# Optimization experiments

Hardware: AMD Instinct MI355X
Metric: run time of the kernel (lower is better)

The kernel has to match this reference:

```python
import jax, jax.numpy as jnp
import numpy as np

# Dims (match init_kwargs): d_model=1024, H=16 heads, hd=64, lift=2 -> Nlift=128, top-k t=32
B, T, D = 1, 2048, 1024
H, HD, LIFT, TK = 16, 64, 2, 32
N = LIFT * HD  # 128 lifted dims per head
EPS = 1e-12


def topk_sparsify(x, k):
    """ReLU then keep only the top-k values per last-dim row (rest zeroed).
    Mathematically identical to the torch COO top-k construction: the sparse
    matrix equals the dense matrix with non-top-k entries zeroed."""
    x = jax.nn.relu(x)
    vals, idx = jax.lax.top_k(x, k)              # (..., k)
    n = x.shape[-1]
    flat_idx = idx.reshape(-1, k)
    flat_vals = vals.reshape(-1, k)
    R = flat_idx.shape[0]
    out = jnp.zeros((R, n), dtype=x.dtype)
    out = out.at[jnp.arange(R)[:, None], flat_idx].set(flat_vals)
    return out.reshape(x.shape)


def setup_inputs() -> dict:
    key = jax.random.key(0)
    ks = jax.random.split(key, 6)
    x = jax.random.normal(ks[0], (B, T, D), jnp.float32)
    W_q = jax.random.normal(ks[1], (H * N, D), jnp.float32) * 0.02
    W_k = jax.random.normal(ks[2], (H * N, D), jnp.float32) * 0.02
    W_v = jax.random.normal(ks[3], (H * HD, D), jnp.float32) * 0.02
    W_o = jax.random.normal(ks[4], (D, H * HD), jnp.float32) * 0.02
    sink = jax.random.normal(ks[5], (H, HD), jnp.float32) * 0.02
    log_beta = jnp.zeros((), jnp.float32)
    return {"x": x, "W_q": W_q, "W_k": W_k, "W_v": W_v, "W_o": W_o,
            "sink": sink, "log_beta": log_beta}


def reference(x, W_q, W_k, W_v, W_o, sink, log_beta):
    # Projections (Linear with no bias: x @ W.T)
    q = (x @ W_q.T).reshape(B, T, H, N)
    k = (x @ W_k.T).reshape(B, T, H, N)
    v = (x @ W_v.T).reshape(B, T, H, HD)

    # ReLU + top-k sparsification of lifted Q/K rows
    qs = topk_sparsify(q, TK).transpose(0, 2, 1, 3)  # (B,H,T,N)
    kk = topk_sparsify(k, TK).transpose(0, 2, 1, 3)  # (B,H,T,N)

    # A = Qs @ Ks^T per (batch, head) block; spspmm only produces same-block
    # entries, so the per-head batched matmul is the exact dense equivalent.
    A = jnp.einsum('bhin,bhjn->bhij', qs, kk)        # (B,H,T,T), all >= 0

    # Causal filter: keep j <= i
    causal = jnp.tril(jnp.ones((T, T), dtype=bool))
    A = jnp.where(causal, A, jnp.zeros((), A.dtype))

    # p=1 normalization with learned sink mass beta
    denom = A.sum(-1)                                # (B,H,T)
    beta = jnp.exp(log_beta)
    denom_ws = denom + beta
    A = A / jnp.maximum(denom_ws, EPS)[..., None]

    vh = v.transpose(0, 2, 1, 3)                     # (B,H,T,HD)
    Y = jnp.einsum('bhij,bhjd->bhid', A, vh)         # (B,H,T,HD)
    Y = Y + (beta / denom_ws)[..., None] * sink[None, :, None, :]

    Y = Y.transpose(0, 2, 1, 3).reshape(B, T, H * HD)
    return Y @ W_o.T
```

## Files before the change

### kernel.cpp

```cpp
#include <hip/hip_runtime.h>

typedef __attribute__((ext_vector_type(8))) short bf8v;
typedef __attribute__((ext_vector_type(4))) float f4v;
typedef unsigned short u16;
typedef unsigned int   u32;
#define AS1 __attribute__((address_space(1)))
#define AS3 __attribute__((address_space(3)))

__device__ inline u16 f2b(float f){
  u32 u = __builtin_bit_cast(u32, f);
  u += 0x7fffu + ((u >> 16) & 1u);
  return (u16)(u >> 16);
}

__global__ __launch_bounds__(256) void conv_all(const float* __restrict__ x,  const float* __restrict__ wq,
                                                const float* __restrict__ wk, const float* __restrict__ wv,
                                                const float* __restrict__ wo,
                                                u16* xb, u16* wqb, u16* wkb, u16* wvb, u16* wob){
  int i = blockIdx.x * 256 + threadIdx.x;
  const float* src; u16* dst; int off;
  if      (i <  524288){ src = x;  dst = xb;  off = i; }
  else if (i < 1048576){ src = wq; dst = wqb; off = i -  524288; }
  else if (i < 1572864){ src = wk; dst = wkb; off = i - 1048576; }
  else if (i < 1835008){ src = wv; dst = wvb; off = i - 1572864; }
  else                 { src = wo; dst = wob; off = i - 1835008; }
  float4 v = ((const float4*)src)[off];
  uint2 r;
  r.x = (u32)f2b(v.x) | ((u32)f2b(v.y) << 16);
  r.y = (u32)f2b(v.z) | ((u32)f2b(v.w) << 16);
  ((uint2*)dst)[off] = r;
}

template<int NFR>
__device__ __forceinline__ void gemm_core(const u16* __restrict__ A, const u16* __restrict__ B,
                                          int K, int m0, int n0, u16* lds, f4v (&acc)[4][NFR]){
  const int tid = threadIdx.x;
  const int l = tid & 63, w = tid >> 6;
  const int wrow = (w >> 1) * 64, wcol = (w & 1) * (NFR * 16);
  constexpr int SB = 4096 + NFR * 1024;
  #pragma unroll
  for (int a = 0; a < 4; a++)
    #pragma unroll
    for (int b = 0; b < NFR; b++) acc[a][b] = (f4v)0.0f;

  const int lrow = l >> 2;
  const int lseg = l & 3;

  auto stage = [&](int k0, int buf){
    u16* At = lds + buf * SB;
    u16* Bt = At + 4096;
    #pragma unroll
    for (int j = 0; j < 2; j++){
      int ca = w * 2 + j;
      int row = ca * 16 + lrow;
      int sseg = (lseg ^ ((row >> 1) & 3)) * 8;
      __builtin_amdgcn_global_load_lds((const AS1 void*)(A + (size_t)(m0 + row) * K + k0 + sseg),
                                       (AS3 void*)(At + ca * 512), 16, 0, 0);
    }
    #pragma unroll
    for (int j = 0; j < NFR / 2; j++){
      int cb = w * (NFR / 2) + j;
      int row = cb * 16 + lrow;
      int sseg = (lseg ^ ((row >> 1) & 3)) * 8;
      __builtin_amdgcn_global_load_lds((const AS1 void*)(B + (size_t)(n0 + row) * K + k0 + sseg),
                                       (AS3 void*)(Bt + cb * 512), 16, 0, 0);
    }
  };

  stage(0, 0);
  __syncthreads();
  int buf = 0;
  for (int k0 = 0; k0 < K; k0 += 32){
    if (k0 + 32 < K) stage(k0 + 32, buf ^ 1);
    const u16* At = lds + buf * SB;
    const u16* Bt = At + 4096;
    bf8v af[4], bfr[NFR];
    #pragma unroll
    for (int mr = 0; mr < 4; mr++){
      int row = wrow + mr * 16 + (l & 15);
      af[mr] = *(const bf8v*)(At + row * 32 + (((l >> 4) ^ ((row >> 1) & 3)) * 8));
    }
    #pragma unroll
    for (int nc = 0; nc < NFR; nc++){
      int row = wcol + nc * 16 + (l & 15);
      bfr[nc] = *(const bf8v*)(Bt + row * 32 + (((l >> 4) ^ ((row >> 1) & 3)) * 8));
    }
    #pragma unroll
    for (int mr = 0; mr < 4; mr++)
      #pragma unroll
      for (int nc = 0; nc < NFR; nc++)
        acc[mr][nc] = __builtin_amdgcn_mfma_f32_16x16x32_bf16(af[mr], bfr[nc], acc[mr][nc], 0, 0, 0);
    __syncthreads();
    buf ^= 1;
  }
}

__global__ __launch_bounds__(256, 4) void qkv_gemm(const u16* __restrict__ xb,
                                                   const u16* __restrict__ wqb, const u16* __restrict__ wkb,
                                                   const u16* __restrict__ wvb,
                                                   u16* qf, u16* kf, u16* vtb){
  __shared__ u16 lds[16384];
  int b = (blockIdx.x & 7) * 80 + (blockIdx.x >> 3);
  const u16* Bp; int which;
  if (b < 256)      { Bp = wqb; which = 0; }
  else if (b < 512) { Bp = wkb; which = 1; b -= 256; }
  else              { Bp = wvb; which = 2; b -= 512; }
  int sh = (which == 2) ? 3 : 4;
  int m0 = (b >> sh) * 128, n0 = (b & ((1 << sh) - 1)) * 128;

  f4v acc[4][4];
  gemm_core<4>(xb, Bp, 1024, m0, n0, lds, acc);

  const int l = threadIdx.x & 63, w = threadIdx.x >> 6;
  const int wrow = (w >> 1) * 64, wcol = (w & 1) * 64;
  if (which < 2){
    u16* C = which ? kf : qf;
    #pragma unroll
    for (int mr = 0; mr < 4; mr++)
      #pragma unroll
      for (int nc = 0; nc < 4; nc++)
        #pragma unroll
        for (int rr = 0; rr < 4; rr++){
          int row = m0 + wrow + mr * 16 + (l >> 4) * 4 + rr;
          int col = n0 + wcol + nc * 16 + (l & 15);
          C[(size_t)row * 2048 + col] = f2b(acc[mr][nc][rr]);
        }
  } else {
    #pragma unroll
    for (int mr = 0; mr < 4; mr++)
      #pragma unroll
      for (int nc = 0; nc < 4; nc++){
        int gcol = n0 + wcol + nc * 16 + (l & 15);
        int t0 = m0 + wrow + mr * 16 + (l >> 4) * 4;
        uint2 pk;
        pk.x = (u32)f2b(acc[mr][nc][0]) | ((u32)f2b(acc[mr][nc][1]) << 16);
        pk.y = (u32)f2b(acc[mr][nc][2]) | ((u32)f2b(acc[mr][nc][3]) << 16);
        *(uint2*)(vtb + (size_t)gcol * 2048 + t0) = pk;
      }
  }
}

__global__ __launch_bounds__(256, 4) void o_gemm(const u16* __restrict__ yb, const u16* __restrict__ wob,
                                                 float* out){
  __shared__ u16 lds[12288];
  int b = (blockIdx.x & 7) * 32 + (blockIdx.x >> 3);
  int m0 = (b >> 4) * 128, n0 = (b & 15) * 64;
  f4v acc[4][2];
  gemm_core<2>(yb, wob, 1024, m0, n0, lds, acc);
  const int l = threadIdx.x & 63, w = threadIdx.x >> 6;
  const int wrow = (w >> 1) * 64, wcol = (w & 1) * 32;
  #pragma unroll
  for (int mr = 0; mr < 4; mr++)
    #pragma unroll
    for (int nc = 0; nc < 2; nc++)
      #pragma unroll
      for (int rr = 0; rr < 4; rr++){
        int row = m0 + wrow + mr * 16 + (l >> 4) * 4 + rr;
        int col = n0 + wcol + nc * 16 + (l & 15);
        out[(size_t)row * 1024 + col] = acc[mr][nc][rr];
      }
}

__global__ __launch_bounds__(256) void topk2(const u16* __restrict__ qf, const u16* __restrict__ kf,
                                             u16* __restrict__ qsb, u16* __restrict__ ksb){
  int w = threadIdx.x >> 6, l = threadIdx.x & 63;
  int b = blockIdx.x;
  const u16* src; u16* dst;
  if (b < 2048){ src = qf; dst = qsb; } else { src = kf; dst = ksb; b -= 2048; }
  int base = b * 16 + w * 4;
  u32 u0[4], u1[4], pre[4];
  int tt[4], hh[4];
  #pragma unroll
  for (int j = 0; j < 4; j++){
    int r = base + j;
    tt[j] = r >> 4; hh[j] = r & 15;
    u32 pair = ((const u32*)(src + (size_t)tt[j] * 2048 + hh[j] * 128))[l];
    u0[j] = pair & 0xFFFFu; u1[j] = pair >> 16;
    if (u0[j] & 0x8000u) u0[j] = 0;
    if (u1[j] & 0x8000u) u1[j] = 0;
    pre[j] = 0;
  }
  for (int bb = 14; bb >= 0; --bb){
    #pragma unroll
    for (int j = 0; j < 4; j++){
      u32 cand = pre[j] | (1u << bb);
      int c = __builtin_popcountll(__ballot(u0[j] >= cand)) + __builtin_popcountll(__ballot(u1[j] >= cand));
      if (c >= 32) pre[j] = cand;
    }
  }
  #pragma unroll
  for (int j = 0; j < 4; j++){
    u32 o0 = (u0[j] >= pre[j]) ? u0[j] : 0u;
    u32 o1 = (u1[j] >= pre[j]) ? u1[j] : 0u;
    ((u32*)(dst + ((size_t)hh[j] * 2048 + tt[j]) * 128))[l] = o0 | (o1 << 16);
  }
}

__global__ __launch_bounds__(512, 6) void attn3(const u16* __restrict__ qs, const u16* __restrict__ ks,
                                                const u16* __restrict__ vt, const float* __restrict__ sink,
                                                const float* __restrict__ logbeta, u16* __restrict__ yout,
                                                float* __restrict__ Yp, float* __restrict__ Dp){
  __shared__ u16 Kt[8192];
  __shared__ u16 Vt[2][4096];
  __shared__ u16 St[8][16 * 72];
  const int tid = threadIdx.x, l = tid & 63, w = tid >> 6;
  const int b = blockIdx.x;
  const int slot = b >> 3;
  const int h = (b & 7) + 8 * (slot / 40);
  const int u = slot % 40;
  int it, chunk, nch;
  if (u < 4)       { it = u; chunk = 0; nch = 1; }
  else if (u < 12) { it = 4 + ((u - 4) >> 1);  chunk = (u - 4) & 1;  nch = 2; }
  else if (u < 24) { it = 8 + (u - 12) / 3;    chunk = (u - 12) % 3; nch = 3; }
  else             { it = 12 + ((u - 24) >> 2); chunk = (u - 24) & 3; nch = 4; }
  const int tiles = 2 * it + 2;
  const int jt0 = (tiles * chunk) / nch;
  const int jt1 = (tiles * (chunk + 1)) / nch;
  const int qrow0 = it * 128 + w * 16;
  const float beta = expf(logbeta[0]);

  bf8v qfr[4];
  {
    int trow = qrow0 + (l & 15);
    const u16* qrow = qs + ((size_t)h * 2048 + trow) * 128 + (l >> 4) * 8;
    #pragma unroll
    for (int kk = 0; kk < 4; kk++) qfr[kk] = *(const bf8v*)(qrow + kk * 32);
  }

  f4v accY[4];
  #pragma unroll
  for (int c = 0; c < 4; c++) accY[c] = (f4v)0.0f;
  float dsum[4] = {0.f, 0.f, 0.f, 0.f};

  const u16* kroot = ks + (size_t)h * 2048 * 128;
  const u16* vroot = vt + (size_t)h * 64 * 2048;

  auto stageK = [&](int jt){
    const u16* kbase = kroot + (size_t)jt * 64 * 128;
    #pragma unroll
    for (int i = 0; i < 2; i++){
      int g = i * 512 + tid;
      int r = g >> 4, c = g & 15;
      __builtin_amdgcn_global_load_lds((const AS1 void*)(kbase + r * 128 + (c ^ (r & 7)) * 8),
                                       (AS3 void*)(&Kt[(i * 512 + w * 64) * 8]), 16, 0, 0);
    }
  };
  auto stageV = [&](int jt, int b2){
    int d = tid >> 3, c = tid & 7;
    __builtin_amdgcn_global_load_lds((const AS1 void*)(vroot + (size_t)d * 2048 + jt * 64 + (c ^ (d & 7)) * 8),
                                     (AS3 void*)(&Vt[b2][w * 512]), 16, 0, 0);
  };

  stageK(jt0);
  stageV(jt0, 0);
  __syncthreads();
  int buf = 0;
  for (int jt = jt0; jt < jt1; ++jt){
    bool pf = (jt + 1 < jt1);
    if (pf) stageV(jt + 1, buf ^ 1);
    const bool act = (jt * 64 <= qrow0 + 15);

    f4v accS[4];
    if (act){
      #pragma unroll
      for (int c = 0; c < 4; c++) accS[c] = (f4v)0.0f;
      __builtin_amdgcn_s_setprio(1);
      #pragma unroll
      for (int c = 0; c < 4; c++){
        int r = c * 16 + (l & 15);
        #pragma unroll
        for (int kk = 0; kk < 4; kk++){
          int ch = kk * 4 + (l >> 4);
          bf8v kfr = *(const bf8v*)(&Kt[r * 128 + ((ch ^ (r & 7)) * 8)]);
          accS[c] = __builtin_amdgcn_mfma_f32_16x16x32_bf16(qfr[kk], kfr, accS[c], 0, 0, 0);
        }
      }
      __builtin_amdgcn_s_setprio(0);
    }
    __builtin_amdgcn_s_barrier();
    __builtin_amdgcn_sched_barrier(0);
    if (pf) stageK(jt + 1);

    if (act){
      if (jt * 64 + 63 > qrow0){
        #pragma unroll
        for (int c = 0; c < 4; c++)
          #pragma unroll
          for (int rr = 0; rr < 4; rr++){
            int i = qrow0 + (l >> 4) * 4 + rr;
            int j = jt * 64 + c * 16 + (l & 15);
            if (j > i) accS[c][rr] = 0.f;
          }
      }
      #pragma unroll
      for (int c = 0; c < 4; c++)
        #pragma unroll
        for (int rr = 0; rr < 4; rr++){
          dsum[rr] += accS[c][rr];
          St[w][((l >> 4) * 4 + rr) * 72 + c * 16 + (l & 15)] = f2b(accS[c][rr]);
        }
      __builtin_amdgcn_s_setprio(1);
      #pragma unroll
      for (int k2 = 0; k2 < 2; k2++){
        bf8v afr = *(const bf8v*)(&St[w][(l & 15) * 72 + k2 * 32 + (l >> 4) * 8]);
        #pragma unroll
        for (int c = 0; c < 4; c++){
          int d = c * 16 + (l & 15);
          int ch = k2 * 4 + (l >> 4);
          bf8v vfr = *(const bf8v*)(&Vt[buf][d * 64 + ((ch ^ (d & 7)) * 8)]);
          accY[c] = __builtin_amdgcn_mfma_f32_16x16x32_bf16(afr, vfr, accY[c], 0, 0, 0);
        }
      }
      __builtin_amdgcn_s_setprio(0);
    }
    __syncthreads();
    buf ^= 1;
  }

  #pragma unroll
  for (int rr = 0; rr < 4; rr++){
    float s = dsum[rr];
    s += __shfl_xor(s, 1, 64);
    s += __shfl_xor(s, 2, 64);
    s += __shfl_xor(s, 4, 64);
    s += __shfl_xor(s, 8, 64);
    dsum[rr] = s;
  }

  if (nch == 1){
    #pragma unroll
    for (int c = 0; c < 4; c++){
      float sv = sink[h * 64 + c * 16 + (l & 15)];
      #pragma unroll
      for (int rr = 0; rr < 4; rr++){
        float den = dsum[rr] + beta;
        float inv = 1.0f / fmaxf(den, 1e-12f);
        float y = (accY[c][rr] + beta * sv) * inv;
        int row = qrow0 + (l >> 4) * 4 + rr;
        yout[(size_t)row * 1024 + h * 64 + c * 16 + (l & 15)] = f2b(y);
      }
    }
  } else {
    float* yp = Yp + ((size_t)h * 40 + u) * 8192;
    #pragma unroll
    for (int c = 0; c < 4; c++)
      #pragma unroll
      for (int rr = 0; rr < 4; rr++){
        int rowib = w * 16 + (l >> 4) * 4 + rr;
        yp[rowib * 64 + c * 16 + (l & 15)] = accY[c][rr];
      }
    if ((l & 15) == 0){
      #pragma unroll
      for (int rr = 0; rr < 4; rr++)
        Dp[((size_t)h * 40 + u) * 128 + w * 16 + (l >> 4) * 4 + rr] = dsum[rr];
    }
  }
}

__global__ __launch_bounds__(256) void attn_reduce(const float* __restrict__ Yp, const float* __restrict__ Dp,
                                                   const float* __restrict__ sink, const float* __restrict__ logbeta,
                                                   u16* __restrict__ yout){
  int blk = blockIdx.x;
  int h = blk / 12, it = 4 + blk % 12;
  int nch = it / 4 + 1;
  int u0 = (it < 8) ? 4 + (it - 4) * 2 : (it < 12) ? 12 + (it - 8) * 3 : 24 + (it - 12) * 4;
  float beta = expf(logbeta[0]);
  __shared__ float inv_s[128];
  int t = threadIdx.x;
  if (t < 128){
    float s = 0.f;
    for (int c = 0; c < nch; c++) s += Dp[((size_t)h * 40 + u0 + c) * 128 + t];
    inv_s[t] = 1.0f / fmaxf(s + beta, 1e-12f);
  }
  __syncthreads();
  const float* base = Yp + ((size_t)h * 40 + u0) * 8192;
  #pragma unroll
  for (int e = 0; e < 32; e++){
    int idx = e * 256 + t;
    float acc = 0.f;
    for (int c = 0; c < nch; c++) acc += base[c * 8192 + idx];
    int row = idx >> 6, col = idx & 63;
    float y = (acc + beta * sink[h * 64 + col]) * inv_s[row];
    yout[(size_t)(it * 128 + row) * 1024 + h * 64 + col] = f2b(y);
  }
}

extern "C" void kernel_launch(void* const* d_in, const int* in_sizes, int n_in,
                              void* d_out, int out_size, void* d_ws, size_t ws_size,
                              hipStream_t stream){
  const float* x    = (const float*)d_in[0];
  const float* Wq   = (const float*)d_in[1];
  const float* Wk   = (const float*)d_in[2];
  const float* Wv   = (const float*)d_in[3];
  const float* Wo   = (const float*)d_in[4];
  const float* sink = (const float*)d_in[5];
  const float* logb = (const float*)d_in[6];

  char* ws = (char*)d_ws;
  u16*   xb  = (u16*)(ws + 0);
  u16*   wqb = (u16*)(ws + 4194304);
  u16*   wkb = (u16*)(ws + 8388608);
  u16*   wvb = (u16*)(ws + 12582912);
  u16*   wob = (u16*)(ws + 14680064);
  u16*   qf  = (u16*)(ws + 16777216);
  u16*   kf  = (u16*)(ws + 33554432);
  u16*   qsb = (u16*)(ws + 50331648);
  u16*   ksb = (u16*)(ws + 58720256);
  u16*   vtb = (u16*)(ws + 67108864);
  u16*   yb  = (u16*)(ws + 71303168);
  float* Yp  = (float*)(ws + 16777216);
  float* Dp  = (float*)(ws + 37748736);

  conv_all<<<8192, 256, 0, stream>>>(x, Wq, Wk, Wv, Wo, xb, wqb, wkb, wvb, wob);
  qkv_gemm<<<640, 256, 0, stream>>>(xb, wqb, wkb, wvb, qf, kf, vtb);
  topk2<<<4096, 256, 0, stream>>>(qf, kf, qsb, ksb);
  attn3<<<640, 512, 0, stream>>>(qsb, ksb, vtb, sink, logb, yb, Yp, Dp);
  attn_reduce<<<192, 256, 0, stream>>>(Yp, Dp, sink, logb, yb);
  o_gemm<<<256, 256, 0, stream>>>(yb, wob, (float*)d_out);
}
```

Measured before the change: 136.9 us.

## Fuse split-K attention reduction into attn3 via last-block atomic counter

Removes the separate attn_reduce kernel. Each split chunk block increments a per-(head, query tile) atomic counter after writing its partial Y and denominators, and the last block to arrive sums the partials, normalizes and writes bf16 output. The partial buffers are compacted to cover only split tiles, and a memset clears the counters each call. This saves a kernel launch and its scheduling gap, at the cost of thread fences, an atomic, and tail work done serially inside the attention kernel.

```diff
diff --git a/kernel.cpp b/kernel.cpp
--- a/kernel.cpp
+++ b/kernel.cpp
@@ -199,10 +199,13 @@
 __global__ __launch_bounds__(512, 6) void attn3(const u16* __restrict__ qs, const u16* __restrict__ ks,
                                                 const u16* __restrict__ vt, const float* __restrict__ sink,
                                                 const float* __restrict__ logbeta, u16* __restrict__ yout,
-                                                float* __restrict__ Yp, float* __restrict__ Dp){
+                                                float* __restrict__ Yp, float* __restrict__ Dp,
+                                                int* __restrict__ Cnt){
   __shared__ u16 Kt[8192];
   __shared__ u16 Vt[2][4096];
   __shared__ u16 St[8][16 * 72];
+  __shared__ int isLast;
+  __shared__ float inv_s[128];
   const int tid = threadIdx.x, l = tid & 63, w = tid >> 6;
   const int b = blockIdx.x;
   const int slot = b >> 3;
@@ -341,7 +344,8 @@
       }
     }
   } else {
-    float* yp = Yp + ((size_t)h * 40 + u) * 8192;
+    const int slotIdx = h * 36 + (u - 4);
+    float* yp = Yp + (size_t)slotIdx * 8192;
     #pragma unroll
     for (int c = 0; c < 4; c++)
       #pragma unroll
@@ -352,36 +356,35 @@
     if ((l & 15) == 0){
       #pragma unroll
       for (int rr = 0; rr < 4; rr++)
-        Dp[((size_t)h * 40 + u) * 128 + w * 16 + (l >> 4) * 4 + rr] = dsum[rr];
-    }
-  }
-}
-
-__global__ __launch_bounds__(256) void attn_reduce(const float* __restrict__ Yp, const float* __restrict__ Dp,
-                                                   const float* __restrict__ sink, const float* __restrict__ logbeta,
-                                                   u16* __restrict__ yout){
-  int blk = blockIdx.x;
-  int h = blk / 12, it = 4 + blk % 12;
-  int nch = it / 4 + 1;
-  int u0 = (it < 8) ? 4 + (it - 4) * 2 : (it < 12) ? 12 + (it - 8) * 3 : 24 + (it - 12) * 4;
-  float beta = expf(logbeta[0]);
-  __shared__ float inv_s[128];
-  int t = threadIdx.x;
-  if (t < 128){
-    float s = 0.f;
-    for (int c = 0; c < nch; c++) s += Dp[((size_t)h * 40 + u0 + c) * 128 + t];
-    inv_s[t] = 1.0f / fmaxf(s + beta, 1e-12f);
-  }
-  __syncthreads();
-  const float* base = Yp + ((size_t)h * 40 + u0) * 8192;
-  #pragma unroll
-  for (int e = 0; e < 32; e++){
-    int idx = e * 256 + t;
-    float acc = 0.f;
-    for (int c = 0; c < nch; c++) acc += base[c * 8192 + idx];
-    int row = idx >> 6, col = idx & 63;
-    float y = (acc + beta * sink[h * 64 + col]) * inv_s[row];
-    yout[(size_t)(it * 128 + row) * 1024 + h * 64 + col] = f2b(y);
+        Dp[(size_t)slotIdx * 128 + w * 16 + (l >> 4) * 4 + rr] = dsum[rr];
+    }
+    __threadfence();
+    __syncthreads();
+    if (tid == 0){
+      int old = atomicAdd(&Cnt[h * 12 + (it - 4)], 1);
+      isLast = (old == nch - 1) ? 1 : 0;
+    }
+    __syncthreads();
+    if (isLast){
+      __threadfence();
+      int s0 = h * 36 + ((it < 8) ? (it - 4) * 2 : (it < 12) ? 8 + (it - 8) * 3 : 20 + (it - 12) * 4);
+      if (tid < 128){
+        float s = 0.f;
+        for (int c = 0; c < nch; c++) s += Dp[(size_t)(s0 + c) * 128 + tid];
+        inv_s[tid] = 1.0f / fmaxf(s + beta, 1e-12f);
+      }
+      __syncthreads();
+      const float* base = Yp + (size_t)s0 * 8192;
+      #pragma unroll
+      for (int e = 0; e < 16; e++){
+        int idx = e * 512 + tid;
+        float a2 = 0.f;
+        for (int c = 0; c < nch; c++) a2 += base[c * 8192 + idx];
+        int row = idx >> 6, col = idx & 63;
+        float y = (a2 + beta * sink[h * 64 + col]) * inv_s[row];
+        yout[(size_t)(it * 128 + row) * 1024 + h * 64 + col] = f2b(y);
+      }
+    }
   }
 }
 
@@ -409,12 +412,13 @@
   u16*   vtb = (u16*)(ws + 67108864);
   u16*   yb  = (u16*)(ws + 71303168);
   float* Yp  = (float*)(ws + 16777216);
-  float* Dp  = (float*)(ws + 37748736);
-
+  float* Dp  = (float*)(ws + 41943040);
+  int*   Cnt = (int*)(ws + 42237952);
+
+  hipMemsetAsync(Cnt, 0, 192 * sizeof(int), stream);
   conv_all<<<8192, 256, 0, stream>>>(x, Wq, Wk, Wv, Wo, xb, wqb, wkb, wvb, wob);
   qkv_gemm<<<640, 256, 0, stream>>>(xb, wqb, wkb, wvb, qf, kf, vtb);
   topk2<<<4096, 256, 0, stream>>>(qf, kf, qsb, ksb);
-  attn3<<<640, 512, 0, stream>>>(qsb, ksb, vtb, sink, logb, yb, Yp, Dp);
-  attn_reduce<<<192, 256, 0, stream>>>(Yp, Dp, sink, logb, yb);
+  attn3<<<640, 512, 0, stream>>>(qsb, ksb, vtb, sink, logb, yb, Yp, Dp, Cnt);
   o_gemm<<<256, 256, 0, stream>>>(yb, wob, (float*)d_out);
 }
```

After: 319.4 us. 133% more time.
